# Optimization experiments

Hardware: AMD Instinct MI355X
Metric: run time of the kernel (lower is better)

Reference implementation:

```python
import jax, jax.numpy as jnp
import numpy as np
import math

S, D = 8192, 128

def setup_inputs() -> dict:
    key = jax.random.key(0)
    kq, kk, kv = jax.random.split(key, 3)
    return {
        "q": jax.random.normal(kq, (S, D), dtype=jnp.float32),
        "k": jax.random.normal(kk, (S, D), dtype=jnp.float32),
        "v": jax.random.normal(kv, (S, D), dtype=jnp.float32),
    }

def reference(q, k, v):
    # scores: [S, S]; scale by sqrt(d) as in the torch module
    scale = 1.0 / math.sqrt(q.shape[1])
    scores = (q @ k.T) * scale
    attn = jax.nn.softmax(scores, axis=-1)
    return attn @ v
```

## Files before the change

kernel.cpp:

```cpp
#include <hip/hip_runtime.h>
#include <hip/hip_bf16.h>

#define SEQ 8192
#define HD 128
#define BM 128
#define BN 64
#define NQT (SEQ / BM)
#define THREADS 512

typedef __bf16 bf16_t;
typedef __bf16 bf16x8 __attribute__((ext_vector_type(8)));
typedef float f32x4 __attribute__((ext_vector_type(4)));

#if __has_builtin(__builtin_amdgcn_exp2f)
__device__ inline float exp2_fast(float x) { return __builtin_amdgcn_exp2f(x); }
#else
__device__ inline float exp2_fast(float x) { return exp2f(x); }
#endif

__global__ __launch_bounds__(256) void prep_kernel(const float* __restrict__ K,
                                                   const float* __restrict__ V,
                                                   bf16_t* __restrict__ Kb,
                                                   bf16_t* __restrict__ VT) {
  const int b = (int)blockIdx.x;
  const int tid = (int)threadIdx.x;
  if (b < 256) {
    __shared__ float tile[64][65];
    const int s0 = (b & 127) * 64;
    const int d0 = (b >> 7) * 64;
    const int r = tid >> 2;
    const int c0 = (tid & 3) * 16;
#pragma unroll
    for (int j4 = 0; j4 < 4; ++j4) {
      float4 x = *(const float4*)&V[(size_t)(s0 + r) * HD + d0 + c0 + j4 * 4];
      tile[r][c0 + j4 * 4 + 0] = x.x;
      tile[r][c0 + j4 * 4 + 1] = x.y;
      tile[r][c0 + j4 * 4 + 2] = x.z;
      tile[r][c0 + j4 * 4 + 3] = x.w;
    }
    __syncthreads();
    bf16x8 w0, w1;
#pragma unroll
    for (int j = 0; j < 8; ++j) w0[j] = (bf16_t)tile[c0 + j][r];
#pragma unroll
    for (int j = 0; j < 8; ++j) w1[j] = (bf16_t)tile[c0 + 8 + j][r];
    *(bf16x8*)&VT[(size_t)(d0 + r) * SEQ + s0 + c0] = w0;
    *(bf16x8*)&VT[(size_t)(d0 + r) * SEQ + s0 + c0 + 8] = w1;
  } else {
    const int base = (b - 256) * 8192 + tid;
#pragma unroll
    for (int j = 0; j < 32; ++j) {
      int i = base + j * 256;
      Kb[i] = (bf16_t)K[i];
    }
  }
}

__global__ __launch_bounds__(THREADS, 4) void fattn_kernel(
    const float* __restrict__ Q, const bf16_t* __restrict__ Kb,
    const bf16_t* __restrict__ VT, float* __restrict__ Opart,
    float* __restrict__ Lpart, int kshift, int nit) {
  __shared__ __align__(16) bf16_t kt[BN][136];
  __shared__ __align__(16) bf16_t vt[HD][72];
  __shared__ __align__(16) bf16_t pt[8][16][72];

  const int tid = (int)threadIdx.x;
  const int lane = tid & 63;
  const int w = tid >> 6;
  const int quad = lane >> 4;
  const int ml = lane & 15;

  const int qt = (int)blockIdx.x >> kshift;
  const int sp = (int)blockIdx.x & ((1 << kshift) - 1);
  const int qbase = qt * BM;
  const int kbase0 = sp * (nit * BN);

  const float SC2 = 0.08838834764831845f * 1.4426950408889634f;

  bf16x8 qf[4];
  {
    const float* qp = Q + (size_t)(qbase + w * 16 + ml) * HD + quad * 8;
#pragma unroll
    for (int kk = 0; kk < 4; ++kk) {
      float4 a = *(const float4*)(qp + kk * 32);
      float4 b = *(const float4*)(qp + kk * 32 + 4);
      bf16x8 f;
      f[0] = (bf16_t)a.x; f[1] = (bf16_t)a.y; f[2] = (bf16_t)a.z; f[3] = (bf16_t)a.w;
      f[4] = (bf16_t)b.x; f[5] = (bf16_t)b.y; f[6] = (bf16_t)b.z; f[7] = (bf16_t)b.w;
      qf[kk] = f;
    }
  }

  f32x4 o_acc[8];
#pragma unroll
  for (int i = 0; i < 8; ++i)
#pragma unroll
    for (int e = 0; e < 4; ++e) o_acc[i][e] = 0.f;
  float l_part[4] = {0.f, 0.f, 0.f, 0.f};

  for (int it = 0; it < nit; ++it) {
    const int kbase = kbase0 + it * BN;
#pragma unroll
    for (int j = 0; j < 2; ++j) {
      int ch = tid + j * THREADS;
      int r = ch >> 4;
      int c8 = (ch & 15) * 8;
      *(bf16x8*)&kt[r][c8] = *(const bf16x8*)&Kb[(size_t)(kbase + r) * HD + c8];
    }
#pragma unroll
    for (int j = 0; j < 2; ++j) {
      int ch = tid + j * THREADS;
      int d = ch >> 3;
      int c8 = (ch & 7) * 8;
      *(bf16x8*)&vt[d][c8] = *(const bf16x8*)&VT[(size_t)d * SEQ + kbase + c8];
    }
    __syncthreads();

    f32x4 sacc[4];
#pragma unroll
    for (int nt = 0; nt < 4; ++nt)
#pragma unroll
      for (int e = 0; e < 4; ++e) sacc[nt][e] = 0.f;
#pragma unroll
    for (int kk = 0; kk < 4; ++kk) {
#pragma unroll
      for (int nt = 0; nt < 4; ++nt) {
        bf16x8 bfr = *(const bf16x8*)&kt[nt * 16 + ml][kk * 32 + quad * 8];
        sacc[nt] = __builtin_amdgcn_mfma_f32_16x16x32_bf16(qf[kk], bfr, sacc[nt], 0, 0, 0);
      }
    }

#pragma unroll
    for (int nt = 0; nt < 4; ++nt) {
#pragma unroll
      for (int r = 0; r < 4; ++r) {
        float p = exp2_fast(sacc[nt][r] * SC2);
        l_part[r] += p;
        pt[w][quad * 4 + r][nt * 16 + ml] = (bf16_t)p;
      }
    }

#pragma unroll
    for (int kk = 0; kk < 2; ++kk) {
      bf16x8 pa = *(const bf16x8*)&pt[w][ml][kk * 32 + quad * 8];
#pragma unroll
      for (int ot = 0; ot < 8; ++ot) {
        bf16x8 vb = *(const bf16x8*)&vt[ot * 16 + ml][kk * 32 + quad * 8];
        o_acc[ot] = __builtin_amdgcn_mfma_f32_16x16x32_bf16(pa, vb, o_acc[ot], 0, 0, 0);
      }
    }
    __syncthreads();
  }

  {
    float* op = Opart + ((size_t)sp * SEQ + qbase + w * 16) * HD;
#pragma unroll
    for (int ot = 0; ot < 8; ++ot)
#pragma unroll
      for (int r = 0; r < 4; ++r)
        op[(quad * 4 + r) * HD + ot * 16 + ml] = o_acc[ot][r];
#pragma unroll
    for (int r = 0; r < 4; ++r) {
      float v = l_part[r];
      v += __shfl_xor(v, 1);
      v += __shfl_xor(v, 2);
      v += __shfl_xor(v, 4);
      v += __shfl_xor(v, 8);
      l_part[r] = v;
    }
    if (ml == 0) {
#pragma unroll
      for (int r = 0; r < 4; ++r)
        Lpart[(size_t)sp * SEQ + qbase + w * 16 + quad * 4 + r] = l_part[r];
    }
  }
}

__global__ __launch_bounds__(256) void combine_kernel(const float* __restrict__ Opart,
                                                      const float* __restrict__ Lpart,
                                                      float* __restrict__ out, int ksplit) {
  const int tid = (int)threadIdx.x;
  const int row = (int)blockIdx.x * 8 + (tid >> 5);
  const int c0 = (tid & 31) * 4;
  float lsum = 0.f;
  for (int s = 0; s < ksplit; ++s) lsum += Lpart[(size_t)s * SEQ + row];
  f32x4 acc;
#pragma unroll
  for (int e = 0; e < 4; ++e) acc[e] = 0.f;
  for (int s = 0; s < ksplit; ++s) {
    f32x4 o = *(const f32x4*)&Opart[((size_t)s * SEQ + row) * HD + c0];
#pragma unroll
    for (int e = 0; e < 4; ++e) acc[e] += o[e];
  }
  const float inv = 1.0f / lsum;
  f32x4 res;
#pragma unroll
  for (int e = 0; e < 4; ++e) res[e] = acc[e] * inv;
  *(f32x4*)&out[(size_t)row * HD + c0] = res;
}

extern "C" void kernel_launch(void* const* d_in, const int* in_sizes, int n_in,
                              void* d_out, int out_size, void* d_ws, size_t ws_size,
                              hipStream_t stream) {
  const float* Q = (const float*)d_in[0];
  const float* K = (const float*)d_in[1];
  const float* V = (const float*)d_in[2];
  float* out = (float*)d_out;

  int ksplit = 8, kshift = 3;
  while (ksplit > 1) {
    size_t need = (size_t)ksplit * SEQ * HD * 4
                + (size_t)ksplit * SEQ * 4
                + (size_t)SEQ * HD * 2 * 2;
    if (need <= ws_size) break;
    ksplit >>= 1; kshift--;
  }

  char* ws = (char*)d_ws;
  float* Opart = (float*)ws;
  float* Lpart = (float*)(ws + (size_t)ksplit * SEQ * HD * 4);
  bf16_t* Kb = (bf16_t*)(ws + (size_t)ksplit * SEQ * HD * 4 + (size_t)ksplit * SEQ * 4);
  bf16_t* VT = Kb + (size_t)SEQ * HD;

  const int nit = SEQ / (ksplit * BN);

  prep_kernel<<<384, 256, 0, stream>>>(K, V, Kb, VT);
  fattn_kernel<<<NQT * ksplit, THREADS, 0, stream>>>(Q, Kb, VT, Opart, Lpart, kshift, nit);
  combine_kernel<<<SEQ / 8, 256, 0, stream>>>(Opart, Lpart, out, ksplit);
}
```

Before: 131.8 us.

## Switch attention to 32x32x16 MFMA with 4 waves and register-staged K/V loads

Replaces the 16x16x32 bf16 MFMA tiling with 32x32x16 MFMA, so each of 4 waves (256 threads) owns 32 query rows instead of 8 waves owning 16. K/V tiles are now loaded into registers before the barrier and written to LDS after it, which lets global loads overlap the previous iteration's compute. LDS paddings change and the K bf16 conversion is vectorised to 8 elements per thread. The larger per-wave accumulator state raises register pressure, and occupancy is lowered to 2 blocks per SM in the launch bounds.

```diff
diff --git a/kernel.cpp b/kernel.cpp
--- a/kernel.cpp
+++ b/kernel.cpp
@@ -6,11 +6,15 @@
 #define BM 128
 #define BN 64
 #define NQT (SEQ / BM)
-#define THREADS 512
+#define THREADS 256
+#define KTP 130
+#define VTP 66
+#define PTP 66
 
 typedef __bf16 bf16_t;
 typedef __bf16 bf16x8 __attribute__((ext_vector_type(8)));
 typedef float f32x4 __attribute__((ext_vector_type(4)));
+typedef float f32x16 __attribute__((ext_vector_type(16)));
 
 #if __has_builtin(__builtin_amdgcn_exp2f)
 __device__ inline float exp2_fast(float x) { return __builtin_amdgcn_exp2f(x); }
@@ -47,28 +51,29 @@
     *(bf16x8*)&VT[(size_t)(d0 + r) * SEQ + s0 + c0] = w0;
     *(bf16x8*)&VT[(size_t)(d0 + r) * SEQ + s0 + c0 + 8] = w1;
   } else {
-    const int base = (b - 256) * 8192 + tid;
-#pragma unroll
-    for (int j = 0; j < 32; ++j) {
-      int i = base + j * 256;
-      Kb[i] = (bf16_t)K[i];
-    }
-  }
-}
-
-__global__ __launch_bounds__(THREADS, 4) void fattn_kernel(
+    const int base = (b - 256) * 2048 + tid * 8;
+    float4 a = *(const float4*)&K[base];
+    float4 c = *(const float4*)&K[base + 4];
+    bf16x8 f;
+    f[0] = (bf16_t)a.x; f[1] = (bf16_t)a.y; f[2] = (bf16_t)a.z; f[3] = (bf16_t)a.w;
+    f[4] = (bf16_t)c.x; f[5] = (bf16_t)c.y; f[6] = (bf16_t)c.z; f[7] = (bf16_t)c.w;
+    *(bf16x8*)&Kb[base] = f;
+  }
+}
+
+__global__ __launch_bounds__(THREADS, 2) void fattn_kernel(
     const float* __restrict__ Q, const bf16_t* __restrict__ Kb,
     const bf16_t* __restrict__ VT, float* __restrict__ Opart,
     float* __restrict__ Lpart, int kshift, int nit) {
-  __shared__ __align__(16) bf16_t kt[BN][136];
-  __shared__ __align__(16) bf16_t vt[HD][72];
-  __shared__ __align__(16) bf16_t pt[8][16][72];
+  __shared__ __align__(16) bf16_t kt[BN][KTP];
+  __shared__ __align__(16) bf16_t vt[HD][VTP];
+  __shared__ __align__(16) bf16_t pt[4][32][PTP];
 
   const int tid = (int)threadIdx.x;
   const int lane = tid & 63;
   const int w = tid >> 6;
-  const int quad = lane >> 4;
-  const int ml = lane & 15;
+  const int h = lane >> 5;
+  const int n32 = lane & 31;
 
   const int qt = (int)blockIdx.x >> kshift;
   const int sp = (int)blockIdx.x & ((1 << kshift) - 1);
@@ -77,13 +82,18 @@
 
   const float SC2 = 0.08838834764831845f * 1.4426950408889634f;
 
-  bf16x8 qf[4];
+  const int kr0 = tid >> 4;
+  const int kc8 = (tid & 15) * 8;
+  const int vd0 = tid >> 3;
+  const int vc8 = (tid & 7) * 8;
+
+  bf16x8 qf[8];
   {
-    const float* qp = Q + (size_t)(qbase + w * 16 + ml) * HD + quad * 8;
-#pragma unroll
-    for (int kk = 0; kk < 4; ++kk) {
-      float4 a = *(const float4*)(qp + kk * 32);
-      float4 b = *(const float4*)(qp + kk * 32 + 4);
+    const float* qp = Q + (size_t)(qbase + w * 32 + n32) * HD + h * 8;
+#pragma unroll
+    for (int kk = 0; kk < 8; ++kk) {
+      float4 a = *(const float4*)(qp + kk * 16);
+      float4 b = *(const float4*)(qp + kk * 16 + 4);
       bf16x8 f;
       f[0] = (bf16_t)a.x; f[1] = (bf16_t)a.y; f[2] = (bf16_t)a.z; f[3] = (bf16_t)a.w;
       f[4] = (bf16_t)b.x; f[5] = (bf16_t)b.y; f[6] = (bf16_t)b.z; f[7] = (bf16_t)b.w;
@@ -91,87 +101,93 @@
     }
   }
 
-  f32x4 o_acc[8];
-#pragma unroll
-  for (int i = 0; i < 8; ++i)
-#pragma unroll
-    for (int e = 0; e < 4; ++e) o_acc[i][e] = 0.f;
-  float l_part[4] = {0.f, 0.f, 0.f, 0.f};
+  f32x16 o_acc[4];
+#pragma unroll
+  for (int i = 0; i < 4; ++i)
+#pragma unroll
+    for (int e = 0; e < 16; ++e) o_acc[i][e] = 0.f;
+  float l_acc[16];
+#pragma unroll
+  for (int i = 0; i < 16; ++i) l_acc[i] = 0.f;
 
   for (int it = 0; it < nit; ++it) {
     const int kbase = kbase0 + it * BN;
-#pragma unroll
-    for (int j = 0; j < 2; ++j) {
-      int ch = tid + j * THREADS;
-      int r = ch >> 4;
-      int c8 = (ch & 15) * 8;
-      *(bf16x8*)&kt[r][c8] = *(const bf16x8*)&Kb[(size_t)(kbase + r) * HD + c8];
-    }
-#pragma unroll
-    for (int j = 0; j < 2; ++j) {
-      int ch = tid + j * THREADS;
-      int d = ch >> 3;
-      int c8 = (ch & 7) * 8;
-      *(bf16x8*)&vt[d][c8] = *(const bf16x8*)&VT[(size_t)d * SEQ + kbase + c8];
-    }
+
+    bf16x8 kreg[4], vreg[4];
+#pragma unroll
+    for (int j = 0; j < 4; ++j)
+      kreg[j] = *(const bf16x8*)&Kb[(size_t)(kbase + kr0 + 16 * j) * HD + kc8];
+#pragma unroll
+    for (int j = 0; j < 4; ++j)
+      vreg[j] = *(const bf16x8*)&VT[(size_t)(vd0 + 32 * j) * SEQ + kbase + vc8];
+
     __syncthreads();
-
-    f32x4 sacc[4];
-#pragma unroll
-    for (int nt = 0; nt < 4; ++nt)
-#pragma unroll
-      for (int e = 0; e < 4; ++e) sacc[nt][e] = 0.f;
+#pragma unroll
+    for (int j = 0; j < 4; ++j) *(bf16x8*)&kt[kr0 + 16 * j][kc8] = kreg[j];
+#pragma unroll
+    for (int j = 0; j < 4; ++j) *(bf16x8*)&vt[vd0 + 32 * j][vc8] = vreg[j];
+    __syncthreads();
+
+    f32x16 sacc[2];
+#pragma unroll
+    for (int nt = 0; nt < 2; ++nt)
+#pragma unroll
+      for (int e = 0; e < 16; ++e) sacc[nt][e] = 0.f;
+#pragma unroll
+    for (int kk = 0; kk < 8; ++kk) {
+#pragma unroll
+      for (int nt = 0; nt < 2; ++nt) {
+        bf16x8 b = *(const bf16x8*)&kt[nt * 32 + n32][kk * 16 + h * 8];
+        sacc[nt] = __builtin_amdgcn_mfma_f32_32x32x16_bf16(qf[kk], b, sacc[nt], 0, 0, 0);
+      }
+    }
+
+#pragma unroll
+    for (int nt = 0; nt < 2; ++nt) {
+#pragma unroll
+      for (int reg = 0; reg < 16; ++reg) {
+        float p = exp2_fast(sacc[nt][reg] * SC2);
+        l_acc[reg] += p;
+        const int row = (reg & 3) + 8 * (reg >> 2);
+        pt[w][row + 4 * h][nt * 32 + n32] = (bf16_t)p;
+      }
+    }
+
 #pragma unroll
     for (int kk = 0; kk < 4; ++kk) {
-#pragma unroll
-      for (int nt = 0; nt < 4; ++nt) {
-        bf16x8 bfr = *(const bf16x8*)&kt[nt * 16 + ml][kk * 32 + quad * 8];
-        sacc[nt] = __builtin_amdgcn_mfma_f32_16x16x32_bf16(qf[kk], bfr, sacc[nt], 0, 0, 0);
-      }
-    }
-
-#pragma unroll
-    for (int nt = 0; nt < 4; ++nt) {
-#pragma unroll
-      for (int r = 0; r < 4; ++r) {
-        float p = exp2_fast(sacc[nt][r] * SC2);
-        l_part[r] += p;
-        pt[w][quad * 4 + r][nt * 16 + ml] = (bf16_t)p;
-      }
-    }
-
-#pragma unroll
-    for (int kk = 0; kk < 2; ++kk) {
-      bf16x8 pa = *(const bf16x8*)&pt[w][ml][kk * 32 + quad * 8];
-#pragma unroll
-      for (int ot = 0; ot < 8; ++ot) {
-        bf16x8 vb = *(const bf16x8*)&vt[ot * 16 + ml][kk * 32 + quad * 8];
-        o_acc[ot] = __builtin_amdgcn_mfma_f32_16x16x32_bf16(pa, vb, o_acc[ot], 0, 0, 0);
-      }
-    }
-    __syncthreads();
+      bf16x8 pa = *(const bf16x8*)&pt[w][n32][kk * 16 + h * 8];
+#pragma unroll
+      for (int ot = 0; ot < 4; ++ot) {
+        bf16x8 vb = *(const bf16x8*)&vt[ot * 32 + n32][kk * 16 + h * 8];
+        o_acc[ot] = __builtin_amdgcn_mfma_f32_32x32x16_bf16(pa, vb, o_acc[ot], 0, 0, 0);
+      }
+    }
   }
 
   {
-    float* op = Opart + ((size_t)sp * SEQ + qbase + w * 16) * HD;
-#pragma unroll
-    for (int ot = 0; ot < 8; ++ot)
-#pragma unroll
-      for (int r = 0; r < 4; ++r)
-        op[(quad * 4 + r) * HD + ot * 16 + ml] = o_acc[ot][r];
-#pragma unroll
-    for (int r = 0; r < 4; ++r) {
-      float v = l_part[r];
+    float* op = Opart + ((size_t)sp * SEQ + qbase + w * 32) * HD;
+#pragma unroll
+    for (int ot = 0; ot < 4; ++ot)
+#pragma unroll
+      for (int reg = 0; reg < 16; ++reg) {
+        const int row = (reg & 3) + 8 * (reg >> 2) + 4 * h;
+        op[row * HD + ot * 32 + n32] = o_acc[ot][reg];
+      }
+#pragma unroll
+    for (int reg = 0; reg < 16; ++reg) {
+      float v = l_acc[reg];
       v += __shfl_xor(v, 1);
       v += __shfl_xor(v, 2);
       v += __shfl_xor(v, 4);
       v += __shfl_xor(v, 8);
-      l_part[r] = v;
-    }
-    if (ml == 0) {
-#pragma unroll
-      for (int r = 0; r < 4; ++r)
-        Lpart[(size_t)sp * SEQ + qbase + w * 16 + quad * 4 + r] = l_part[r];
+      v += __shfl_xor(v, 16);
+      l_acc[reg] = v;
+    }
+    if (n32 == 0) {
+      float* lp = Lpart + (size_t)sp * SEQ + qbase + w * 32;
+#pragma unroll
+      for (int reg = 0; reg < 16; ++reg)
+        lp[(reg & 3) + 8 * (reg >> 2) + 4 * h] = l_acc[reg];
     }
   }
 }
@@ -224,7 +240,7 @@
 
   const int nit = SEQ / (ksplit * BN);
 
-  prep_kernel<<<384, 256, 0, stream>>>(K, V, Kb, VT);
+  prep_kernel<<<768, 256, 0, stream>>>(K, V, Kb, VT);
   fattn_kernel<<<NQT * ksplit, THREADS, 0, stream>>>(Q, Kb, VT, Opart, Lpart, kshift, nit);
   combine_kernel<<<SEQ / 8, 256, 0, stream>>>(Opart, Lpart, out, ksplit);
 }
```

Result: faster. 122.6 us (-6.9%).
